# Optimization experiments

Measured on AMD Instinct MI355X. Metric: run time of the kernel, lower is better.

The kernel has to match this reference:

```python
import jax, jax.numpy as jnp
import numpy as np

B, S, H, E = 8, 2048, 1024, 8

def setup_inputs() -> dict:
    key = jax.random.key(0)
    ks = jax.random.split(key, 7)
    sc = 1.0 / np.sqrt(H)
    return {
        "x":   jax.random.normal(ks[0], (B, S, H), dtype=jnp.float32),
        "We":  jax.random.normal(ks[1], (E, H, H), dtype=jnp.float32) * sc,
        "be":  jax.random.normal(ks[2], (E, H), dtype=jnp.float32) * 0.01,
        "Wr1": jax.random.normal(ks[3], (H, H), dtype=jnp.float32) * sc,
        "br1": jax.random.normal(ks[4], (H,), dtype=jnp.float32) * 0.01,
        "Wr2": jax.random.normal(ks[5], (H, E), dtype=jnp.float32) * sc,
        "br2": jax.random.normal(ks[6], (E,), dtype=jnp.float32) * 0.01,
    }

def reference(x, We, be, Wr1, br1, Wr2, br2):
    # Router: mean over seq -> Linear+ReLU -> Linear -> softmax over experts
    x_mean = x.mean(axis=1)                                   # [B,H]
    h = jax.nn.relu(x_mean @ Wr1 + br1)                        # [B,H]
    routing = jax.nn.softmax(h @ Wr2 + br2, axis=-1)           # [B,E]
    # Dense all-experts MLP: every expert processes every token
    eo = jax.nn.relu(jnp.einsum('bsh,ehd->ebsd', x, We)
                     + be[:, None, None, :])                   # [E,B,S,H]
    # KV caches are zero-initialized and read before any update in the
    # original forward, so their additive contribution is zero here.
    out = jnp.einsum('ebsd,be->bsd', eo, routing)              # [B,S,H]
    return out
```

## Files before the change

kernel.cpp:

```cpp
#include <hip/hip_runtime.h>
#include <stdint.h>

#define Hdim 1024
#define Bdim 8
#define Sdim 2048
#define Edim 8
#define Mtot 16384
#define Ntot 8192

typedef short bf16x8 __attribute__((ext_vector_type(8)));
typedef unsigned short u16x8 __attribute__((ext_vector_type(8)));
typedef float f32x4 __attribute__((ext_vector_type(4)));

__device__ __forceinline__ unsigned short f2bf(float f) {
  union { float f; unsigned u; } v; v.f = f;
  unsigned r = (v.u + 0x7FFFu + ((v.u >> 16) & 1u)) >> 16;
  return (unsigned short)r;
}

__device__ __forceinline__ void gload16(const void* g, void* l) {
  __builtin_amdgcn_global_load_lds((const __attribute__((address_space(1))) void*)g,
                                   (__attribute__((address_space(3))) void*)l,
                                   16, 0, 0);
}

#define VMCNT_(N) asm volatile("s_waitcnt vmcnt(" #N ")" ::: "memory")
#define VMCNT(N) VMCNT_(N)
#define LGKM_(N) asm volatile("s_waitcnt lgkmcnt(" #N ")" ::: "memory")
#define LGKM(N) LGKM_(N)
#define SCHED0() __builtin_amdgcn_sched_barrier(0)
#define BAR() __builtin_amdgcn_s_barrier()

__global__ void k_convert_mean(const float* __restrict__ x,
                               unsigned short* __restrict__ xb,
                               float* __restrict__ part) {
  const int b = blockIdx.y;
  const int s0 = blockIdx.x * 32;
  const int t = threadIdx.x;
  const int hg = (t & 127) << 3;
  const int sp = t >> 7;
  float accv[8];
#pragma unroll
  for (int q = 0; q < 8; ++q) accv[q] = 0.f;
#pragma unroll 4
  for (int i = 0; i < 16; ++i) {
    const int s = s0 + sp + (i << 1);
    const size_t base = ((size_t)b * Sdim + s) * Hdim + hg;
    const float4 lo = *(const float4*)(x + base);
    const float4 hi = *(const float4*)(x + base + 4);
    accv[0] += lo.x; accv[1] += lo.y; accv[2] += lo.z; accv[3] += lo.w;
    accv[4] += hi.x; accv[5] += hi.y; accv[6] += hi.z; accv[7] += hi.w;
    u16x8 pk;
    pk[0] = f2bf(lo.x); pk[1] = f2bf(lo.y); pk[2] = f2bf(lo.z); pk[3] = f2bf(lo.w);
    pk[4] = f2bf(hi.x); pk[5] = f2bf(hi.y); pk[6] = f2bf(hi.z); pk[7] = f2bf(hi.w);
    *(u16x8*)(xb + base) = pk;
  }
  float* pp = part + ((size_t)b * 128 + blockIdx.x * 2 + sp) * Hdim + hg;
#pragma unroll
  for (int q = 0; q < 8; ++q) pp[q] = accv[q];
}

__global__ void k_transpose_w(const float* __restrict__ We,
                              unsigned short* __restrict__ wt) {
  __shared__ float lds[64][65];
  const int e = blockIdx.z, hb = blockIdx.y, db = blockIdx.x;
  const int t = threadIdx.x;
  const float* src = We + ((size_t)e * Hdim + hb * 64) * Hdim + db * 64;
#pragma unroll 4
  for (int it = 0; it < 16; ++it) {
    int idx = it * 256 + t;
    int r = idx >> 6, c = idx & 63;
    lds[r][c] = src[(size_t)r * Hdim + c];
  }
  __syncthreads();
#pragma unroll 4
  for (int it = 0; it < 16; ++it) {
    int idx = it * 256 + t;
    int r = idx >> 6, c = idx & 63;
    const int np = (db * 64 + r) * 8 + e;
    wt[(size_t)np * Hdim + hb * 64 + c] = f2bf(lds[c][r]);
  }
}

__global__ void k_router1(const float* __restrict__ part,
                          const float* __restrict__ Wr1,
                          const float* __restrict__ br1,
                          float* __restrict__ hbuf) {
  __shared__ float xm[Hdim];
  const int b = blockIdx.y, jc = blockIdx.x, t = threadIdx.x;
  for (int k = t; k < Hdim; k += 256) {
    float s = 0.f;
    const float* p = part + (size_t)b * 128 * Hdim + k;
#pragma unroll 8
    for (int c = 0; c < 128; ++c) s += p[(size_t)c * Hdim];
    xm[k] = s * (1.0f / 2048.0f);
  }
  __syncthreads();
  const int j = jc * 256 + t;
  float acc = br1[j];
#pragma unroll 8
  for (int k = 0; k < Hdim; ++k) acc = fmaf(xm[k], Wr1[(size_t)k * Hdim + j], acc);
  hbuf[b * Hdim + j] = fmaxf(acc, 0.f);
}

__global__ void k_router2(const float* __restrict__ hbuf,
                          const float* __restrict__ Wr2,
                          const float* __restrict__ br2,
                          float* __restrict__ routing) {
  const int t = threadIdx.x;
  const int e = t & 7;
  const int b = t >> 3;
  float acc = br2[e];
  const float* hb = hbuf + b * Hdim;
#pragma unroll 8
  for (int k = 0; k < Hdim; ++k) acc = fmaf(hb[k], Wr2[k * Edim + e], acc);
  float m = acc;
  for (int d = 1; d < 8; d <<= 1) m = fmaxf(m, __shfl_xor(m, d, 64));
  float p = __expf(acc - m);
  float s = p;
  for (int d = 1; d < 8; d <<= 1) s += __shfl_xor(s, d, 64);
  routing[t] = p / s;
}

__global__ __launch_bounds__(512, 2)
void k_moe_gemm(const unsigned short* __restrict__ xb,
                const unsigned short* __restrict__ wt,
                const float* __restrict__ be,
                const float* __restrict__ routing,
                float* __restrict__ out) {
  extern __shared__ char smem[];
  const int t = threadIdx.x;
  const int wave = t >> 6, lane = t & 63;
  const int la15 = lane & 15;
  const int wr = wave >> 2;
  const int wcn = wave & 3;

  const int bid = blockIdx.x;
  const int wg = (bid & 7) * 256 + (bid >> 3);
  const int m0 = (wg >> 5) * 256;
  const int n0 = (wg & 31) * 256;

  const int cx = (((lane & 7) ^ (lane >> 3)) << 3);
  const unsigned short* aStage = xb + (size_t)(m0 + wave * 8 + (lane >> 3)) * Hdim + cx;
  const int bRowLoc = ((wave & 3) << 3) + ((wave >> 2) << 6) + (lane >> 3);
  const unsigned short* bStage = wt + (size_t)(n0 + bRowLoc) * Hdim + cx;
  const int aLdsW = wave * 1024;
  const int bLdsW = ((wave & 3) << 10) + ((wave >> 2) << 13);

  const int swz0 = (((lane >> 4) ^ (lane & 7)) << 4);
  const int swz1 = ((((lane >> 4) + 4) ^ (lane & 7)) << 4);
  const int aRd = (wr * 128 + la15) * 128;
  const int bRd = (wcn * 64 + la15) * 128;

  f32x4 acc[8][4];
#pragma unroll
  for (int i = 0; i < 8; ++i)
#pragma unroll
    for (int j = 0; j < 4; ++j) acc[i][j] = (f32x4){0.f, 0.f, 0.f, 0.f};

  bf16x8 a0[4][2], a1[4][2], b0[2][2], b1[2][2];

#define STG_A(half, buf, k0) do { \
    gload16(aStage + (half) * 64 * 1024 + (k0),          smem + (buf) * 32768 + aLdsW + (half) * 8192); \
    gload16(aStage + (128 + (half) * 64) * 1024 + (k0),  smem + (buf) * 32768 + aLdsW + 16384 + (half) * 8192); \
  } while (0)
#define STG_B(sub, buf, k0) do { \
    gload16(bStage + (sub) * 32 * 1024 + (k0),           smem + 65536 + (buf) * 32768 + bLdsW + (sub) * 4096); \
    gload16(bStage + (128 + (sub) * 32) * 1024 + (k0),   smem + 65536 + (buf) * 32768 + bLdsW + 16384 + (sub) * 4096); \
  } while (0)
#define LD_A(dst, buf, qi) do { \
    _Pragma("unroll") for (int ii = 0; ii < 4; ++ii) { \
      dst[ii][0] = *(const bf16x8*)(smem + (buf) * 32768 + aRd + (qi) * 8192 + ii * 2048 + swz0); \
      dst[ii][1] = *(const bf16x8*)(smem + (buf) * 32768 + aRd + (qi) * 8192 + ii * 2048 + swz1); } \
  } while (0)
#define LD_A_LO(dst, buf, qi) do { \
    _Pragma("unroll") for (int ii = 0; ii < 2; ++ii) { \
      dst[ii][0] = *(const bf16x8*)(smem + (buf) * 32768 + aRd + (qi) * 8192 + ii * 2048 + swz0); \
      dst[ii][1] = *(const bf16x8*)(smem + (buf) * 32768 + aRd + (qi) * 8192 + ii * 2048 + swz1); } \
  } while (0)
#define LD_A_HI(dst, buf, qi) do { \
    _Pragma("unroll") for (int ii = 2; ii < 4; ++ii) { \
      dst[ii][0] = *(const bf16x8*)(smem + (buf) * 32768 + aRd + (qi) * 8192 + ii * 2048 + swz0); \
      dst[ii][1] = *(const bf16x8*)(smem + (buf) * 32768 + aRd + (qi) * 8192 + ii * 2048 + swz1); } \
  } while (0)
#define LD_B(dst, buf, qj) do { \
    _Pragma("unroll") for (int jj = 0; jj < 2; ++jj) { \
      dst[jj][0] = *(const bf16x8*)(smem + 65536 + (buf) * 32768 + bRd + (qj) * 4096 + jj * 2048 + swz0); \
      dst[jj][1] = *(const bf16x8*)(smem + 65536 + (buf) * 32768 + bRd + (qj) * 4096 + jj * 2048 + swz1); } \
  } while (0)
#define MF_Q(af_, bf_, qi, jh) do { \
    __builtin_amdgcn_s_setprio(1); \
    _Pragma("unroll") for (int ii = 0; ii < 4; ++ii) \
      _Pragma("unroll") for (int jj = 0; jj < 2; ++jj) { \
        acc[(qi)*4+ii][(jh)*2+jj] = __builtin_amdgcn_mfma_f32_16x16x32_bf16(af_[ii][0], bf_[jj][0], acc[(qi)*4+ii][(jh)*2+jj], 0, 0, 0); \
        acc[(qi)*4+ii][(jh)*2+jj] = __builtin_amdgcn_mfma_f32_16x16x32_bf16(af_[ii][1], bf_[jj][1], acc[(qi)*4+ii][(jh)*2+jj], 0, 0, 0); } \
    __builtin_amdgcn_s_setprio(0); \
  } while (0)

  STG_A(0, 0, 0);
  STG_B(1, 0, 0);
  STG_B(0, 0, 0);
  STG_A(1, 0, 0);
  STG_A(0, 1, 64);
  SCHED0();
  STG_B(1, 1, 64);
  STG_B(0, 1, 64);
  STG_A(1, 1, 64);
  VMCNT(6);
  BAR();
  LD_A(a0, 0, 0);
  SCHED0();
  LD_B(b1, 0, 1);

#pragma unroll 1
  for (int j = 0; j < 8; ++j) {
    const int k2 = (j * 128 + 128) & 1023;
    const int k3 = (j * 128 + 192) & 1023;
    LD_B(b0, 0, 0);
    SCHED0();
    LD_A_LO(a1, 0, 1);
    STG_A(0, 0, k2);
    BAR(); LGKM(4); SCHED0();
    MF_Q(a0, b0, 0, 0);
    BAR();
    LD_A_HI(a1, 0, 1);
    STG_B(0, 0, k2);
    BAR(); SCHED0();
    MF_Q(a0, b1, 0, 1);
    BAR();
    LD_A(a0, 1, 0);
    STG_B(1, 0, k2);
    VMCNT(4);
    BAR(); LGKM(8); SCHED0();
    MF_Q(a1, b1, 1, 1);
    BAR();
    LD_B(b1, 1, 1);
    STG_A(1, 0, k2);
    BAR(); SCHED0();
    MF_Q(a1, b0, 1, 0);
    BAR();
    LD_B(b0, 1, 0);
    SCHED0();
    LD_A_LO(a1, 1, 1);
    STG_A(0, 1, k3);
    BAR(); LGKM(4); SCHED0();
    MF_Q(a0, b0, 0, 0);
    BAR();
    LD_A_HI(a1, 1, 1);
    STG_B(0, 1, k3);
    BAR(); SCHED0();
    MF_Q(a0, b1, 0, 1);
    BAR();
    LD_A(a0, 0, 0);
    STG_B(1, 1, k3);
    VMCNT(4);
    BAR(); LGKM(8); SCHED0();
    MF_Q(a1, b1, 1, 1);
    BAR();
    LD_B(b1, 0, 1);
    STG_A(1, 1, k3);
    BAR(); SCHED0();
    MF_Q(a1, b0, 1, 0);
    BAR();
  }

  VMCNT(0);
  BAR();

  float* outb = (float*)smem;
  const int bidx = m0 >> 11;
  const float rw = routing[bidx * Edim + (lane & 7)];
  const int dblk = (lane >> 3) & 1;
  const bool writer = ((lane & 7) == 0);
#pragma unroll
  for (int j = 0; j < 4; ++j) {
    const int col0 = wcn * 64 + j * 16;
    const float bias = be[(lane & 7) * Hdim + (n0 >> 3) + (col0 >> 3) + dblk];
#pragma unroll
    for (int i = 0; i < 8; ++i) {
#pragma unroll
      for (int r = 0; r < 4; ++r) {
        float v = fmaxf(acc[i][j][r] + bias, 0.f) * rw;
        v += __shfl_xor(v, 1, 64);
        v += __shfl_xor(v, 2, 64);
        v += __shfl_xor(v, 4, 64);
        if (writer) {
          const int row = wr * 128 + i * 16 + ((lane >> 4) << 2) + r;
          outb[row * 33 + (col0 >> 3) + dblk] = v;
        }
      }
    }
  }
  BAR();
  const size_t obase = (size_t)m0 * Hdim + (n0 >> 3);
#pragma unroll
  for (int it = 0; it < 4; ++it) {
    const int r = it * 64 + (t >> 3);
    const int c = (t & 7) * 4;
    float4 vv;
    vv.x = outb[r * 33 + c];
    vv.y = outb[r * 33 + c + 1];
    vv.z = outb[r * 33 + c + 2];
    vv.w = outb[r * 33 + c + 3];
    *(float4*)(out + obase + (size_t)r * Hdim + c) = vv;
  }
#undef STG_A
#undef STG_B
#undef LD_A
#undef LD_A_LO
#undef LD_A_HI
#undef LD_B
#undef MF_Q
}

extern "C" void kernel_launch(void* const* d_in, const int* in_sizes, int n_in,
                              void* d_out, int out_size, void* d_ws, size_t ws_size,
                              hipStream_t stream) {
  const float* x   = (const float*)d_in[0];
  const float* We  = (const float*)d_in[1];
  const float* be  = (const float*)d_in[2];
  const float* Wr1 = (const float*)d_in[3];
  const float* br1 = (const float*)d_in[4];
  const float* Wr2 = (const float*)d_in[5];
  const float* br2 = (const float*)d_in[6];
  float* out = (float*)d_out;

  char* ws = (char*)d_ws;
  unsigned short* xb = (unsigned short*)ws;
  unsigned short* wt = (unsigned short*)(ws + 33554432);
  float* part    = (float*)(ws + 50331648);
  float* hbuf    = (float*)(ws + 54525952);
  float* routing = (float*)(ws + 54558720);

  hipFuncSetAttribute((const void*)k_moe_gemm,
                      hipFuncAttributeMaxDynamicSharedMemorySize, 131072);

  k_convert_mean<<<dim3(Sdim / 32, Bdim), 256, 0, stream>>>(x, xb, part);
  k_transpose_w<<<dim3(Hdim / 64, Hdim / 64, Edim), 256, 0, stream>>>(We, wt);
  k_router1<<<dim3(Hdim / 256, Bdim), 256, 0, stream>>>(part, Wr1, br1, hbuf);
  k_router2<<<1, 64, 0, stream>>>(hbuf, Wr2, br2, routing);
  k_moe_gemm<<<dim3(2048), 512, 131072, stream>>>(xb, wt, be, routing, out);
}
```

Measured before the change: 464.0 us.

## Split router into parallel mean and matvec kernels, remap GEMM tiles, simplify waits

Splits the router's first kernel into a separate mean-reduction kernel and a split-K matvec kernel, raising the block count from 32 to 128 and 64 so the serial 128-step partial reduction no longer runs in few blocks. Remaps GEMM workgroups so each XCD handles a contiguous band of M rows, aiming for better L2 reuse of activations. It also removes the sched_barrier and lgkmcnt waits and moves the vmcnt waits inside the main loop, which changes how the compiler interleaves LDS reads with MFMA. The looser waits rely on compiler-inserted synchronization and could lose overlap or, if inserted badly, stall more.

```diff
diff --git a/kernel.cpp b/kernel.cpp
--- a/kernel.cpp
+++ b/kernel.cpp
@@ -26,9 +26,6 @@
 
 #define VMCNT_(N) asm volatile("s_waitcnt vmcnt(" #N ")" ::: "memory")
 #define VMCNT(N) VMCNT_(N)
-#define LGKM_(N) asm volatile("s_waitcnt lgkmcnt(" #N ")" ::: "memory")
-#define LGKM(N) LGKM_(N)
-#define SCHED0() __builtin_amdgcn_sched_barrier(0)
 #define BAR() __builtin_amdgcn_s_barrier()
 
 __global__ void k_convert_mean(const float* __restrict__ x,
@@ -82,25 +79,42 @@
   }
 }
 
-__global__ void k_router1(const float* __restrict__ part,
-                          const float* __restrict__ Wr1,
-                          const float* __restrict__ br1,
-                          float* __restrict__ hbuf) {
-  __shared__ float xm[Hdim];
+__global__ void k_mean(const float* __restrict__ part, float* __restrict__ xm) {
+  __shared__ float red[4][64];
+  const int b = blockIdx.y, hc = blockIdx.x, t = threadIdx.x;
+  const int h = hc * 64 + (t & 63), q = t >> 6;
+  float s = 0.f;
+  const float* p = part + ((size_t)b * 128 + q * 32) * Hdim + h;
+#pragma unroll 8
+  for (int c = 0; c < 32; ++c) s += p[(size_t)c * Hdim];
+  red[q][t & 63] = s;
+  __syncthreads();
+  if (t < 64) {
+    float v = (red[0][t] + red[1][t]) + (red[2][t] + red[3][t]);
+    xm[b * Hdim + hc * 64 + t] = v * (1.0f / 2048.0f);
+  }
+}
+
+__global__ void k_r1(const float* __restrict__ xm,
+                     const float* __restrict__ Wr1,
+                     const float* __restrict__ br1,
+                     float* __restrict__ hbuf) {
+  __shared__ float xs[Hdim];
+  __shared__ float hred[2][128];
   const int b = blockIdx.y, jc = blockIdx.x, t = threadIdx.x;
-  for (int k = t; k < Hdim; k += 256) {
-    float s = 0.f;
-    const float* p = part + (size_t)b * 128 * Hdim + k;
+  for (int k = t; k < Hdim; k += 256) xs[k] = xm[b * Hdim + k];
+  __syncthreads();
+  const int j = jc * 128 + (t & 127);
+  const int kh = (t >> 7) * 512;
+  float acc = 0.f;
 #pragma unroll 8
-    for (int c = 0; c < 128; ++c) s += p[(size_t)c * Hdim];
-    xm[k] = s * (1.0f / 2048.0f);
-  }
+  for (int k = 0; k < 512; ++k)
+    acc = fmaf(xs[kh + k], Wr1[(size_t)(kh + k) * Hdim + j], acc);
+  hred[t >> 7][t & 127] = acc;
   __syncthreads();
-  const int j = jc * 256 + t;
-  float acc = br1[j];
-#pragma unroll 8
-  for (int k = 0; k < Hdim; ++k) acc = fmaf(xm[k], Wr1[(size_t)k * Hdim + j], acc);
-  hbuf[b * Hdim + j] = fmaxf(acc, 0.f);
+  if (t < 128)
+    hbuf[b * Hdim + jc * 128 + t] =
+        fmaxf(hred[0][t] + hred[1][t] + br1[jc * 128 + t], 0.f);
 }
 
 __global__ void k_router2(const float* __restrict__ hbuf,
@@ -136,9 +150,12 @@
   const int wcn = wave & 3;
 
   const int bid = blockIdx.x;
-  const int wg = (bid & 7) * 256 + (bid >> 3);
-  const int m0 = (wg >> 5) * 256;
-  const int n0 = (wg & 31) * 256;
+  const int xcd = bid & 7;
+  const int idx = bid >> 3;
+  const int rnd = idx >> 5;
+  const int slot = idx & 31;
+  const int m0 = (xcd * 8 + (slot & 7)) * 256;
+  const int n0 = (rnd * 4 + (slot >> 3)) * 256;
 
   const int cx = (((lane & 7) ^ (lane >> 3)) << 3);
   const unsigned short* aStage = xb + (size_t)(m0 + wave * 8 + (lane >> 3)) * Hdim + cx;
@@ -198,18 +215,16 @@
   } while (0)
 
   STG_A(0, 0, 0);
+  STG_B(0, 0, 0);
   STG_B(1, 0, 0);
-  STG_B(0, 0, 0);
   STG_A(1, 0, 0);
   STG_A(0, 1, 64);
-  SCHED0();
+  STG_B(0, 1, 64);
   STG_B(1, 1, 64);
-  STG_B(0, 1, 64);
   STG_A(1, 1, 64);
-  VMCNT(6);
+  VMCNT(4);
   BAR();
   LD_A(a0, 0, 0);
-  SCHED0();
   LD_B(b1, 0, 1);
 
 #pragma unroll 1
@@ -217,49 +232,47 @@
     const int k2 = (j * 128 + 128) & 1023;
     const int k3 = (j * 128 + 192) & 1023;
     LD_B(b0, 0, 0);
-    SCHED0();
     LD_A_LO(a1, 0, 1);
     STG_A(0, 0, k2);
-    BAR(); LGKM(4); SCHED0();
+    BAR();
     MF_Q(a0, b0, 0, 0);
     BAR();
     LD_A_HI(a1, 0, 1);
     STG_B(0, 0, k2);
-    BAR(); SCHED0();
+    VMCNT(4);
+    BAR();
     MF_Q(a0, b1, 0, 1);
     BAR();
     LD_A(a0, 1, 0);
     STG_B(1, 0, k2);
-    VMCNT(4);
-    BAR(); LGKM(8); SCHED0();
+    BAR();
     MF_Q(a1, b1, 1, 1);
     BAR();
     LD_B(b1, 1, 1);
     STG_A(1, 0, k2);
-    BAR(); SCHED0();
+    BAR();
     MF_Q(a1, b0, 1, 0);
     BAR();
     LD_B(b0, 1, 0);
-    SCHED0();
     LD_A_LO(a1, 1, 1);
     STG_A(0, 1, k3);
-    BAR(); LGKM(4); SCHED0();
+    BAR();
     MF_Q(a0, b0, 0, 0);
     BAR();
     LD_A_HI(a1, 1, 1);
     STG_B(0, 1, k3);
-    BAR(); SCHED0();
+    VMCNT(4);
+    BAR();
     MF_Q(a0, b1, 0, 1);
     BAR();
     LD_A(a0, 0, 0);
     STG_B(1, 1, k3);
-    VMCNT(4);
-    BAR(); LGKM(8); SCHED0();
+    BAR();
     MF_Q(a1, b1, 1, 1);
     BAR();
     LD_B(b1, 0, 1);
     STG_A(1, 1, k3);
-    BAR(); SCHED0();
+    BAR();
     MF_Q(a1, b0, 1, 0);
     BAR();
   }
@@ -329,15 +342,17 @@
   unsigned short* xb = (unsigned short*)ws;
   unsigned short* wt = (unsigned short*)(ws + 33554432);
   float* part    = (float*)(ws + 50331648);
-  float* hbuf    = (float*)(ws + 54525952);
-  float* routing = (float*)(ws + 54558720);
+  float* xm      = (float*)(ws + 54525952);
+  float* hbuf    = (float*)(ws + 54558720);
+  float* routing = (float*)(ws + 54591488);
 
   hipFuncSetAttribute((const void*)k_moe_gemm,
                       hipFuncAttributeMaxDynamicSharedMemorySize, 131072);
 
   k_convert_mean<<<dim3(Sdim / 32, Bdim), 256, 0, stream>>>(x, xb, part);
   k_transpose_w<<<dim3(Hdim / 64, Hdim / 64, Edim), 256, 0, stream>>>(We, wt);
-  k_router1<<<dim3(Hdim / 256, Bdim), 256, 0, stream>>>(part, Wr1, br1, hbuf);
+  k_mean<<<dim3(16, Bdim), 256, 0, stream>>>(part, xm);
+  k_r1<<<dim3(8, Bdim), 256, 0, stream>>>(xm, Wr1, br1, hbuf);
   k_router2<<<1, 64, 0, stream>>>(hbuf, Wr2, br2, routing);
   k_moe_gemm<<<dim3(2048), 512, 131072, stream>>>(xb, wt, be, routing, out);
 }
```

Result: faster. 421.5 us (-9.2%).
